# Kernel optimization log

Measured on AMD Instinct MI355X. Metric: run time of the kernel, lower is better.

## Reference

```python
import jax, jax.numpy as jnp
import numpy as np

DIM = 768
HEADS = 12
HEAD_DIM = DIM // HEADS
EPS = 1e-5


def _layernorm(x, w, b):
    # normalize over last axis (head_dim), affine params shape [head_dim]
    mu = jnp.mean(x, axis=-1, keepdims=True)
    var = jnp.mean(jnp.square(x - mu), axis=-1, keepdims=True)
    return (x - mu) * jax.lax.rsqrt(var + EPS) * w + b


def setup_inputs() -> dict:
    key = jax.random.key(0)
    ks = jax.random.split(key, 8)
    B, N, C = 8, 1024, DIM
    s = 1.0 / np.sqrt(C)
    return {
        "x": jax.random.normal(ks[0], (B, N, C), jnp.float32),
        "qkv_w": jax.random.normal(ks[1], (3 * C, C), jnp.float32) * s,
        "qkv_b": jnp.zeros((3 * C,), jnp.float32),
        "qn_w": jnp.ones((HEAD_DIM,), jnp.float32),
        "qn_b": jnp.zeros((HEAD_DIM,), jnp.float32),
        "kn_w": jnp.ones((HEAD_DIM,), jnp.float32),
        "kn_b": jnp.zeros((HEAD_DIM,), jnp.float32),
        "proj_w": jax.random.normal(ks[2], (C, C), jnp.float32) * s,
        "proj_b": jnp.zeros((C,), jnp.float32),
    }


def reference(x, qkv_w, qkv_b, qn_w, qn_b, kn_w, kn_b, proj_w, proj_b):
    B, N, C = x.shape
    H, D = HEADS, HEAD_DIM
    scale = D ** -0.5
    # qkv projection: [B,N,3C] -> [3,B,H,N,D]
    qkv = (x @ qkv_w.T + qkv_b).reshape(B, N, 3, H, D).transpose(2, 0, 3, 1, 4)
    q, k, v = qkv[0], qkv[1], qkv[2]
    q = _layernorm(q, qn_w, qn_b)
    k = _layernorm(k, kn_w, kn_b)
    # attention scores [B,H,N,N]
    attn = jnp.einsum("bhqd,bhkd->bhqk", q, k) * scale
    attn = jax.nn.softmax(attn, axis=-1)
    out = jnp.einsum("bhqk,bhkd->bhqd", attn, v)  # [B,H,N,D]
    out = out.transpose(0, 2, 1, 3).reshape(B, N, C)
    return out @ proj_w.T + proj_b
```

## Files before the change

### kernel.cpp

```cpp
#include <hip/hip_runtime.h>

#define DIM 768
#define HEADS 12
#define HDIM 64
#define B_ 8
#define N_ 1024
#define EPS 1e-5f
#define QPRE 0.18033688f

typedef __bf16 bf16x8 __attribute__((ext_vector_type(8)));
typedef float  f32x4  __attribute__((ext_vector_type(4)));

using u16 = unsigned short;
using u32 = unsigned int;

static __device__ __forceinline__ u16 f2b_rne(float f){
    u32 u = __float_as_uint(f);
    u += 0x7fffu + ((u >> 16) & 1u);
    return (u16)(u >> 16);
}

static __device__ __forceinline__ u32 cvt_pk_bf16(float lo, float hi){
    u32 r;
    asm("v_cvt_pk_bf16_f32 %0, %1, %2" : "=v"(r) : "v"(lo), "v"(hi));
    return r;
}

static __device__ __forceinline__ void gl_lds16(const void* g, void* l){
    __builtin_amdgcn_global_load_lds(
        (const __attribute__((address_space(1))) unsigned int*)g,
        (__attribute__((address_space(3))) unsigned int*)l, 16, 0, 0);
}

__global__ __launch_bounds__(256) void cast_bf16_kernel(
    const float* __restrict__ in, u16* __restrict__ out, int n8)
{
    int i = blockIdx.x * 256 + threadIdx.x;
    if (i >= n8) return;
    const float4* p = (const float4*)in;
    float4 a = p[2*i], b = p[2*i+1];
    uint4 r;
    r.x = (u32)f2b_rne(a.x) | ((u32)f2b_rne(a.y) << 16);
    r.y = (u32)f2b_rne(a.z) | ((u32)f2b_rne(a.w) << 16);
    r.z = (u32)f2b_rne(b.x) | ((u32)f2b_rne(b.y) << 16);
    r.w = (u32)f2b_rne(b.z) | ((u32)f2b_rne(b.w) << 16);
    ((uint4*)out)[i] = r;
}

__global__ __launch_bounds__(256) void qkv_gemm_ln(
    const u16* __restrict__ xb, const u16* __restrict__ wb,
    const float* __restrict__ bias,
    const float* __restrict__ qn_w, const float* __restrict__ qn_b,
    const float* __restrict__ kn_w, const float* __restrict__ kn_b,
    u16* __restrict__ Q, u16* __restrict__ K, u16* __restrict__ VT)
{
    __shared__ __align__(16) unsigned char Asl[128*128];
    __shared__ __align__(16) unsigned char Bsl[128*128];
    const int t = threadIdx.x;
    const int lane = t & 63, wid = t >> 6;
    const int wr = wid >> 1, wc = wid & 1;
    const int l15 = lane & 15, l4 = lane >> 4;
    const int lr  = lane >> 3;
    const int lcs = ((lane & 7) ^ lr & 7) * 16;
    const int rsw = (l15 & 7) << 4;

    const int b0 = blockIdx.x;
    const int lg = (b0 & 7) * 144 + (b0 >> 3);
    const int col0 = (lg % 18) * 128, row0 = (lg / 18) * 128;

    f32x4 acc[4][4];
    #pragma unroll
    for (int m = 0; m < 4; ++m)
        #pragma unroll
        for (int n = 0; n < 4; ++n) acc[m][n] = f32x4{0.f,0.f,0.f,0.f};

    for (int k0 = 0; k0 < DIM; k0 += 64) {
        __syncthreads();
        #pragma unroll
        for (int c = 0; c < 4; ++c) {
            int rg = wid*32 + c*8;
            gl_lds16((const unsigned char*)xb + (size_t)(row0 + rg + lr)*1536 + k0*2 + lcs,
                     Asl + rg*128);
            gl_lds16((const unsigned char*)wb + (size_t)(col0 + rg + lr)*1536 + k0*2 + lcs,
                     Bsl + rg*128);
        }
        __syncthreads();
        #pragma unroll
        for (int s = 0; s < 2; ++s) {
            bf16x8 af[4], bfr[4];
            #pragma unroll
            for (int m = 0; m < 4; ++m)
                af[m] = *(const bf16x8*)(Asl + (wr*64 + m*16 + l15)*128 + ((l4*16 + s*64) ^ rsw));
            #pragma unroll
            for (int n = 0; n < 4; ++n)
                bfr[n] = *(const bf16x8*)(Bsl + (wc*64 + n*16 + l15)*128 + ((l4*16 + s*64) ^ rsw));
            #pragma unroll
            for (int m = 0; m < 4; ++m)
                #pragma unroll
                for (int n = 0; n < 4; ++n)
                    acc[m][n] = __builtin_amdgcn_mfma_f32_16x16x32_bf16(af[m], bfr[n], acc[m][n], 0, 0, 0);
        }
    }

    const int cg0 = col0 + wc*64;
    const int which = cg0 / DIM;
    const int h = (cg0 % DIM) / HDIM;

    float bias_v[4];
    #pragma unroll
    for (int n = 0; n < 4; ++n) bias_v[n] = bias[cg0 + n*16 + l15];
    #pragma unroll
    for (int m = 0; m < 4; ++m)
        #pragma unroll
        for (int n = 0; n < 4; ++n)
            #pragma unroll
            for (int r = 0; r < 4; ++r) acc[m][n][r] += bias_v[n];

    __syncthreads();
    unsigned char* Tw = (wid < 2 ? Asl : Bsl) + (wid & 1) * 8192;

    if (which < 2) {
        const float* lwp = (which == 0) ? qn_w : kn_w;
        const float* lbp = (which == 0) ? qn_b : kn_b;
        const float qsc = (which == 0) ? QPRE : 1.0f;
        float lw_v[4], lb_v[4];
        #pragma unroll
        for (int n = 0; n < 4; ++n) { lw_v[n] = lwp[n*16 + l15] * qsc; lb_v[n] = lbp[n*16 + l15] * qsc; }

        #pragma unroll
        for (int m = 0; m < 4; ++m)
            #pragma unroll
            for (int r = 0; r < 4; ++r) {
                float s = 0.f, s2 = 0.f;
                #pragma unroll
                for (int n = 0; n < 4; ++n) { float v = acc[m][n][r]; s += v; s2 += v*v; }
                #pragma unroll
                for (int off = 1; off < 16; off <<= 1) {
                    s  += __shfl_xor(s,  off, 64);
                    s2 += __shfl_xor(s2, off, 64);
                }
                float mu  = s * (1.f/64.f);
                float var = s2 * (1.f/64.f) - mu*mu;
                float rs  = rsqrtf(var + EPS);
                #pragma unroll
                for (int n = 0; n < 4; ++n)
                    acc[m][n][r] = (acc[m][n][r] - mu) * rs * lw_v[n] + lb_v[n];
            }

        #pragma unroll
        for (int m = 0; m < 4; ++m)
            #pragma unroll
            for (int n = 0; n < 4; ++n)
                #pragma unroll
                for (int r = 0; r < 4; ++r)
                    *(u16*)(Tw + (m*16 + l4*4 + r)*128 + (n*16 + l15)*2) = f2b_rne(acc[m][n][r]);

        u16* dst = (which == 0) ? Q : K;
        const int tok0 = row0 + wr*64;
        const int b = tok0 >> 10, n0 = tok0 & 1023;
        const size_t bh = (size_t)(b * HEADS + h);
        #pragma unroll
        for (int i = 0; i < 8; ++i) {
            int row = i*8 + (lane >> 3);
            int d0  = (lane & 7) * 8;
            uint4 val = *(const uint4*)(Tw + row*128 + d0*2);
            *(uint4*)(dst + (bh * N_ + n0 + row) * HDIM + d0) = val;
        }
    } else {
        #pragma unroll
        for (int n = 0; n < 4; ++n)
            #pragma unroll
            for (int m = 0; m < 4; ++m)
                #pragma unroll
                for (int r = 0; r < 4; ++r)
                    *(u16*)(Tw + (n*16 + l15)*128 + (m*16 + l4*4 + r)*2) = f2b_rne(acc[m][n][r]);

        const int tok0 = row0 + wr*64;
        const int b = tok0 >> 10, n0v = tok0 & 1023;
        const size_t bh = (size_t)(b * HEADS + h);
        #pragma unroll
        for (int i = 0; i < 8; ++i) {
            int d  = i*8 + (lane >> 3);
            int tk = (lane & 7) * 8;
            uint4 val = *(const uint4*)(Tw + d*128 + tk*2);
            *(uint4*)(VT + (bh * HDIM + d) * N_ + n0v + tk) = val;
        }
    }
}

__global__ __launch_bounds__(256) void attn_mfma(
    const u16* __restrict__ Q, const u16* __restrict__ K,
    const u16* __restrict__ VT, u16* __restrict__ A)
{
    __shared__ __align__(16) unsigned char Ks[2][64*128];
    __shared__ __align__(16) unsigned char Vs[2][64*128];
    __shared__ __align__(16) unsigned char Ps[4*2176];
    const int t = threadIdx.x, lane = t & 63, w = t >> 6;
    const int l15 = lane & 15, l4 = lane >> 4;
    const int lr  = lane >> 3;
    const int lcs = ((lane & 7) ^ lr & 7) * 16;
    const int rsw = (l15 & 7) << 4;
    const int psw = (l15 & 7) << 4;

    const int b0 = blockIdx.x;
    const int lg = (b0 & 7) * 192 + (b0 >> 3);
    const int qt = lg & 15, bh = lg >> 4;
    const size_t base = (size_t)bh * (N_ * HDIM);

    bf16x8 qa[2];
    {
        const unsigned char* qb = (const unsigned char*)(Q + base + (size_t)(qt*64 + w*16 + l15) * HDIM);
        qa[0] = *(const bf16x8*)(qb + l4*16);
        qa[1] = *(const bf16x8*)(qb + l4*16 + 64);
    }

    float l_run = 0.f;
    f32x4 o[4];
    #pragma unroll
    for (int m = 0; m < 4; ++m) o[m] = f32x4{0.f,0.f,0.f,0.f};

    unsigned char* Pw = Ps + w*2176;

    const unsigned char* kSrc = (const unsigned char*)K  + base*2 + (size_t)(w*16 + lr)*128  + lcs;
    const unsigned char* vSrc = (const unsigned char*)VT + base*2 + (size_t)(w*16 + lr)*2048 + lcs;
    unsigned char* kDst0 = Ks[0] + w*16*128;
    unsigned char* vDst0 = Vs[0] + w*16*128;

    auto stage = [&](int buf, int kt2){
        #pragma unroll
        for (int c = 0; c < 2; ++c) {
            gl_lds16(kSrc + (size_t)kt2*8192 + c*1024,  kDst0 + buf*8192 + c*1024);
            gl_lds16(vSrc + kt2*128 + c*16384,          vDst0 + buf*8192 + c*1024);
        }
    };

    stage(0, 0);
    __syncthreads();

    for (int kt = 0; kt < 16; ++kt) {
        const int cur = kt & 1;
        if (kt < 15) stage(cur ^ 1, kt + 1);

        f32x4 sv[4];
        #pragma unroll
        for (int n = 0; n < 4; ++n) {
            sv[n] = f32x4{0.f,0.f,0.f,0.f};
            #pragma unroll
            for (int s = 0; s < 2; ++s) {
                bf16x8 kb = *(const bf16x8*)(Ks[cur] + (n*16 + l15)*128 + ((l4*16 + s*64) ^ rsw));
                sv[n] = __builtin_amdgcn_mfma_f32_16x16x32_bf16(kb, qa[s], sv[n], 0, 0, 0);
            }
        }

        #pragma unroll
        for (int n = 0; n < 4; ++n) {
            float p0 = exp2f(sv[n][0]), p1 = exp2f(sv[n][1]);
            float p2 = exp2f(sv[n][2]), p3 = exp2f(sv[n][3]);
            l_run += (p0 + p1) + (p2 + p3);
            uint2 pw;
            pw.x = cvt_pk_bf16(p0, p1);
            pw.y = cvt_pk_bf16(p2, p3);
            *(uint2*)(Pw + l15*128 + ((n*32 + l4*8) ^ psw)) = pw;
        }

        #pragma unroll
        for (int s = 0; s < 2; ++s) {
            bf16x8 pb = *(const bf16x8*)(Pw + l15*128 + ((s*64 + l4*16) ^ psw));
            #pragma unroll
            for (int m = 0; m < 4; ++m) {
                bf16x8 vb = *(const bf16x8*)(Vs[cur] + (m*16 + l15)*128 + ((l4*16 + s*64) ^ rsw));
                o[m] = __builtin_amdgcn_mfma_f32_16x16x32_bf16(vb, pb, o[m], 0, 0, 0);
            }
        }

        __syncthreads();
    }

    l_run += __shfl_xor(l_run, 16, 64);
    l_run += __shfl_xor(l_run, 32, 64);
    const float inv = 1.f / l_run;

    const int b = bh / HEADS, h = bh % HEADS;
    #pragma unroll
    for (int m = 0; m < 4; ++m)
        #pragma unroll
        for (int r = 0; r < 4; ++r)
            *(u16*)(Pw + l15*132 + (m*16 + l4*4 + r)*2) = f2b_rne(o[m][r] * inv);
    #pragma unroll
    for (int i = 0; i < 2; ++i) {
        int row = i*8 + (lane >> 3);
        int d0  = (lane & 7) * 8;
        uint4 val = *(const uint4*)(Pw + row*132 + d0*2);
        int tok = qt*64 + w*16 + row;
        *(uint4*)(A + (((size_t)b * N_ + tok) * HEADS + h) * HDIM + d0) = val;
    }
}

__global__ __launch_bounds__(256) void proj_gemm(
    const u16* __restrict__ Ab, const u16* __restrict__ wb,
    const float* __restrict__ bias, float* __restrict__ out)
{
    __shared__ __align__(16) unsigned char Asl[128*128];
    __shared__ __align__(16) unsigned char Bsl[128*128];
    const int t = threadIdx.x;
    const int lane = t & 63, wid = t >> 6;
    const int wr = wid >> 1, wc = wid & 1;
    const int l15 = lane & 15, l4 = lane >> 4;
    const int lr  = lane >> 3;
    const int lcs = ((lane & 7) ^ lr & 7) * 16;
    const int rsw = (l15 & 7) << 4;

    const int b0 = blockIdx.x;
    const int lg = (b0 & 7) * 48 + (b0 >> 3);
    const int col0 = (lg % 6) * 128, row0 = (lg / 6) * 128;

    f32x4 acc[4][4];
    #pragma unroll
    for (int m = 0; m < 4; ++m)
        #pragma unroll
        for (int n = 0; n < 4; ++n) acc[m][n] = f32x4{0.f,0.f,0.f,0.f};

    for (int k0 = 0; k0 < DIM; k0 += 64) {
        __syncthreads();
        #pragma unroll
        for (int c = 0; c < 4; ++c) {
            int rg = wid*32 + c*8;
            gl_lds16((const unsigned char*)Ab + (size_t)(row0 + rg + lr)*1536 + k0*2 + lcs,
                     Asl + rg*128);
            gl_lds16((const unsigned char*)wb + (size_t)(col0 + rg + lr)*1536 + k0*2 + lcs,
                     Bsl + rg*128);
        }
        __syncthreads();
        #pragma unroll
        for (int s = 0; s < 2; ++s) {
            bf16x8 af[4], bfr[4];
            #pragma unroll
            for (int m = 0; m < 4; ++m)
                af[m] = *(const bf16x8*)(Asl + (wr*64 + m*16 + l15)*128 + ((l4*16 + s*64) ^ rsw));
            #pragma unroll
            for (int n = 0; n < 4; ++n)
                bfr[n] = *(const bf16x8*)(Bsl + (wc*64 + n*16 + l15)*128 + ((l4*16 + s*64) ^ rsw));
            #pragma unroll
            for (int m = 0; m < 4; ++m)
                #pragma unroll
                for (int n = 0; n < 4; ++n)
                    acc[m][n] = __builtin_amdgcn_mfma_f32_16x16x32_bf16(af[m], bfr[n], acc[m][n], 0, 0, 0);
        }
    }

    float bias_v[4];
    #pragma unroll
    for (int n = 0; n < 4; ++n) bias_v[n] = bias[col0 + wc*64 + n*16 + l15];
    #pragma unroll
    for (int m = 0; m < 4; ++m)
        #pragma unroll
        for (int r = 0; r < 4; ++r) {
            int rg = row0 + wr*64 + m*16 + l4*4 + r;
            #pragma unroll
            for (int n = 0; n < 4; ++n)
                out[(size_t)rg * DIM + col0 + wc*64 + n*16 + l15] = acc[m][n][r] + bias_v[n];
        }
}

extern "C" void kernel_launch(void* const* d_in, const int* in_sizes, int n_in,
                              void* d_out, int out_size, void* d_ws, size_t ws_size,
                              hipStream_t stream)
{
    const float* x      = (const float*)d_in[0];
    const float* qkv_w  = (const float*)d_in[1];
    const float* qkv_b  = (const float*)d_in[2];
    const float* qn_w   = (const float*)d_in[3];
    const float* qn_b   = (const float*)d_in[4];
    const float* kn_w   = (const float*)d_in[5];
    const float* kn_b   = (const float*)d_in[6];
    const float* proj_w = (const float*)d_in[7];
    const float* proj_b = (const float*)d_in[8];
    float* out = (float*)d_out;

    const size_t XE  = (size_t)B_ * N_ * DIM;
    const size_t QWE = (size_t)3 * DIM * DIM;
    const size_t PWE = (size_t)DIM * DIM;

    u16* xb  = (u16*)d_ws;
    u16* qwb = xb  + XE;
    u16* pwb = qwb + QWE;
    u16* Qb  = pwb + PWE;
    u16* Kb  = Qb  + XE;
    u16* VTb = Kb  + XE;
    u16* Ab  = VTb + XE;

    cast_bf16_kernel<<<(int)((XE/8  + 255)/256), 256, 0, stream>>>(x,      xb,  (int)(XE/8));
    cast_bf16_kernel<<<(int)((QWE/8 + 255)/256), 256, 0, stream>>>(qkv_w,  qwb, (int)(QWE/8));
    cast_bf16_kernel<<<(int)((PWE/8 + 255)/256), 256, 0, stream>>>(proj_w, pwb, (int)(PWE/8));

    qkv_gemm_ln<<<dim3(1152), 256, 0, stream>>>(xb, qwb, qkv_b, qn_w, qn_b,
                                                kn_w, kn_b, Qb, Kb, VTb);
    attn_mfma<<<dim3(1536), 256, 0, stream>>>(Qb, Kb, VTb, Ab);
    proj_gemm<<<dim3(384), 256, 0, stream>>>(Ab, pwb, proj_b, out);
}
```

Measured before the change: 144.9 us.

## Double-buffer LDS tiles in QKV and projection GEMM main loops

Both GEMM kernels now keep two LDS buffers per operand. Each step issues the global-to-LDS loads for the next K tile before computing on the current one, and there is one barrier per iteration instead of two. The goal is to hide global load latency behind MFMA work. LDS use per block doubles to 64KB, which can lower occupancy, and correctness depends on the async load completing by the end-of-iteration barrier.

Measured after the change: 152.7 us. 1.05x slower.

```diff
diff --git a/kernel.cpp b/kernel.cpp
--- a/kernel.cpp
+++ b/kernel.cpp
@@ -54,8 +54,8 @@
     const float* __restrict__ kn_w, const float* __restrict__ kn_b,
     u16* __restrict__ Q, u16* __restrict__ K, u16* __restrict__ VT)
 {
-    __shared__ __align__(16) unsigned char Asl[128*128];
-    __shared__ __align__(16) unsigned char Bsl[128*128];
+    __shared__ __align__(16) unsigned char Asl[2][128*128];
+    __shared__ __align__(16) unsigned char Bsl[2][128*128];
     const int t = threadIdx.x;
     const int lane = t & 63, wid = t >> 6;
     const int wr = wid >> 1, wc = wid & 1;
@@ -74,32 +74,41 @@
         #pragma unroll
         for (int n = 0; n < 4; ++n) acc[m][n] = f32x4{0.f,0.f,0.f,0.f};
 
-    for (int k0 = 0; k0 < DIM; k0 += 64) {
-        __syncthreads();
+    const unsigned char* aSrc = (const unsigned char*)xb + (size_t)(row0 + lr)*1536 + lcs;
+    const unsigned char* bSrc = (const unsigned char*)wb + (size_t)(col0 + lr)*1536 + lcs;
+
+    auto stage = [&](int buf, int k0s){
         #pragma unroll
         for (int c = 0; c < 4; ++c) {
             int rg = wid*32 + c*8;
-            gl_lds16((const unsigned char*)xb + (size_t)(row0 + rg + lr)*1536 + k0*2 + lcs,
-                     Asl + rg*128);
-            gl_lds16((const unsigned char*)wb + (size_t)(col0 + rg + lr)*1536 + k0*2 + lcs,
-                     Bsl + rg*128);
-        }
-        __syncthreads();
+            gl_lds16(aSrc + (size_t)rg*1536 + k0s*2, Asl[buf] + rg*128);
+            gl_lds16(bSrc + (size_t)rg*1536 + k0s*2, Bsl[buf] + rg*128);
+        }
+    };
+
+    stage(0, 0);
+    __syncthreads();
+
+    for (int step = 0; step < 12; ++step) {
+        const int cur = step & 1;
+        if (step < 11) stage(cur ^ 1, (step + 1) * 64);
+
         #pragma unroll
         for (int s = 0; s < 2; ++s) {
             bf16x8 af[4], bfr[4];
             #pragma unroll
             for (int m = 0; m < 4; ++m)
-                af[m] = *(const bf16x8*)(Asl + (wr*64 + m*16 + l15)*128 + ((l4*16 + s*64) ^ rsw));
+                af[m] = *(const bf16x8*)(Asl[cur] + (wr*64 + m*16 + l15)*128 + ((l4*16 + s*64) ^ rsw));
             #pragma unroll
             for (int n = 0; n < 4; ++n)
-                bfr[n] = *(const bf16x8*)(Bsl + (wc*64 + n*16 + l15)*128 + ((l4*16 + s*64) ^ rsw));
+                bfr[n] = *(const bf16x8*)(Bsl[cur] + (wc*64 + n*16 + l15)*128 + ((l4*16 + s*64) ^ rsw));
             #pragma unroll
             for (int m = 0; m < 4; ++m)
                 #pragma unroll
                 for (int n = 0; n < 4; ++n)
                     acc[m][n] = __builtin_amdgcn_mfma_f32_16x16x32_bf16(af[m], bfr[n], acc[m][n], 0, 0, 0);
         }
+        __syncthreads();
     }
 
     const int cg0 = col0 + wc*64;
@@ -116,8 +125,7 @@
             #pragma unroll
             for (int r = 0; r < 4; ++r) acc[m][n][r] += bias_v[n];
 
-    __syncthreads();
-    unsigned char* Tw = (wid < 2 ? Asl : Bsl) + (wid & 1) * 8192;
+    unsigned char* Tw = &Asl[0][0] + wid * 8192;
 
     if (which < 2) {
         const float* lwp = (which == 0) ? qn_w : kn_w;
@@ -300,8 +308,8 @@
     const u16* __restrict__ Ab, const u16* __restrict__ wb,
     const float* __restrict__ bias, float* __restrict__ out)
 {
-    __shared__ __align__(16) unsigned char Asl[128*128];
-    __shared__ __align__(16) unsigned char Bsl[128*128];
+    __shared__ __align__(16) unsigned char Asl[2][128*128];
+    __shared__ __align__(16) unsigned char Bsl[2][128*128];
     const int t = threadIdx.x;
     const int lane = t & 63, wid = t >> 6;
     const int wr = wid >> 1, wc = wid & 1;
@@ -320,32 +328,41 @@
         #pragma unroll
         for (int n = 0; n < 4; ++n) acc[m][n] = f32x4{0.f,0.f,0.f,0.f};
 
-    for (int k0 = 0; k0 < DIM; k0 += 64) {
-        __syncthreads();
+    const unsigned char* aSrc = (const unsigned char*)Ab + (size_t)(row0 + lr)*1536 + lcs;
+    const unsigned char* bSrc = (const unsigned char*)wb + (size_t)(col0 + lr)*1536 + lcs;
+
+    auto stage = [&](int buf, int k0s){
         #pragma unroll
         for (int c = 0; c < 4; ++c) {
             int rg = wid*32 + c*8;
-            gl_lds16((const unsigned char*)Ab + (size_t)(row0 + rg + lr)*1536 + k0*2 + lcs,
-                     Asl + rg*128);
-            gl_lds16((const unsigned char*)wb + (size_t)(col0 + rg + lr)*1536 + k0*2 + lcs,
-                     Bsl + rg*128);
-        }
-        __syncthreads();
+            gl_lds16(aSrc + (size_t)rg*1536 + k0s*2, Asl[buf] + rg*128);
+            gl_lds16(bSrc + (size_t)rg*1536 + k0s*2, Bsl[buf] + rg*128);
+        }
+    };
+
+    stage(0, 0);
+    __syncthreads();
+
+    for (int step = 0; step < 12; ++step) {
+        const int cur = step & 1;
+        if (step < 11) stage(cur ^ 1, (step + 1) * 64);
+
         #pragma unroll
         for (int s = 0; s < 2; ++s) {
             bf16x8 af[4], bfr[4];
             #pragma unroll
             for (int m = 0; m < 4; ++m)
-                af[m] = *(const bf16x8*)(Asl + (wr*64 + m*16 + l15)*128 + ((l4*16 + s*64) ^ rsw));
+                af[m] = *(const bf16x8*)(Asl[cur] + (wr*64 + m*16 + l15)*128 + ((l4*16 + s*64) ^ rsw));
             #pragma unroll
             for (int n = 0; n < 4; ++n)
-                bfr[n] = *(const bf16x8*)(Bsl + (wc*64 + n*16 + l15)*128 + ((l4*16 + s*64) ^ rsw));
+                bfr[n] = *(const bf16x8*)(Bsl[cur] + (wc*64 + n*16 + l15)*128 + ((l4*16 + s*64) ^ rsw));
             #pragma unroll
             for (int m = 0; m < 4; ++m)
                 #pragma unroll
                 for (int n = 0; n < 4; ++n)
                     acc[m][n] = __builtin_amdgcn_mfma_f32_16x16x32_bf16(af[m], bfr[n], acc[m][n], 0, 0, 0);
         }
+        __syncthreads();
     }
 
     float bias_v[4];
```
